# Optimization experiments

Measured on AMD Instinct MI355X. Metric: run time of the kernel, lower is better.

The kernel has to match this reference:

```python
import jax, jax.numpy as jnp
import numpy as np
from jax import lax

N_GAUSS = 8192
SEM_DIM = 32


def setup_inputs() -> dict:
    key = jax.random.key(0)
    k1, k2, k3, k4, k5 = jax.random.split(key, 5)
    H, W = 1024, 1024
    # centers sampled inside the view frustum of an identity-pose pinhole camera
    z = jax.random.uniform(k1, (N_GAUSS,), minval=0.5, maxval=6.0)
    xy = jax.random.uniform(k2, (N_GAUSS, 2), minval=-0.6, maxval=0.6) * z[:, None]
    centers = jnp.concatenate([xy, z[:, None]], axis=1).astype(jnp.float32)
    colors = jax.random.uniform(k3, (N_GAUSS, 3), dtype=jnp.float32)
    opacities = jax.random.uniform(k4, (N_GAUSS, 1), dtype=jnp.float32)
    sem_feats = jax.random.normal(k5, (N_GAUSS, SEM_DIM), dtype=jnp.float32) * 0.1
    camera_pose = jnp.eye(4, dtype=jnp.float32)
    fx = fy = 800.0
    camera_intrinsics = jnp.array([[fx, 0.0, W / 2.0], [0.0, fy, H / 2.0], [0.0, 0.0, 1.0]], dtype=jnp.float32)
    return {
        "centers": centers,
        "colors": colors,
        "opacities": opacities,
        "sem_feats": sem_feats,
        "camera_pose": camera_pose,
        "camera_intrinsics": camera_intrinsics,
        "H": H,
        "W": W,
    }


def reference(centers, colors, opacities, sem_feats, camera_pose, camera_intrinsics, H, W):
    # Differentiable point-splat alpha compositing (faithful to render_gaussians).
    # Torch recurrence per pixel: alpha_i = o_i * (1 - A), A += alpha_i
    # => transmittance before i equals prod_{j<i, same pixel, nearer depth}(1 - o_j).
    N = centers.shape[0]
    cam = centers @ camera_pose[:3, :3].T + camera_pose[:3, 3]  # (N,3)
    z = cam[:, 2]
    valid = z > 0.1
    proj = cam @ camera_intrinsics.T  # (N,3)
    denom = jnp.where(valid, proj[:, 2], 1.0)
    # .long() in torch truncates toward zero; astype(int32) matches for the kept range
    px = (proj[:, 0] / denom).astype(jnp.int32)
    py = (proj[:, 1] / denom).astype(jnp.int32)
    ok = valid & (px >= 0) & (px < W) & (py >= 0) & (py < H)
    pid = jnp.where(ok, py * W + px, H * W)  # invalid -> dump bucket
    o = jnp.where(ok, opacities[:, 0], 0.0)
    depth = jnp.where(ok, z, jnp.inf)
    # sort primarily by pixel, secondarily by depth (front-to-back within pixel)
    order = jnp.lexsort((depth, pid))
    pid_s = pid[order]
    o_s = o[order]
    feats = jnp.concatenate([colors, sem_feats], axis=1)[order]  # (N, 3+D)
    # segmented exclusive cumprod of (1 - o) in log space
    log_t = jnp.log1p(-jnp.clip(o_s, 0.0, 1.0 - 1e-7))
    csum = jnp.cumsum(log_t)
    excl = csum - log_t
    boundary = jnp.concatenate([jnp.array([True]), pid_s[1:] != pid_s[:-1]])
    start_idx = lax.cummax(jnp.where(boundary, jnp.arange(N), 0))
    T = jnp.exp(excl - excl[start_idx])  # transmittance before each splat
    alpha = o_s * T
    out_flat = jax.ops.segment_sum(alpha[:, None] * feats, pid_s, num_segments=H * W + 1)[: H * W]
    feat_dim = feats.shape[1]
    return out_flat.T.reshape(feat_dim, H, W)
```

## Files before the change

kernel.cpp:

```cpp
#include <hip/hip_runtime.h>
#include <stdint.h>

#define CT 4096

__global__ __launch_bounds__(256) void gs_zero_project_kernel(
        float* __restrict__ out, int n,
        const float* __restrict__ centers, const float* __restrict__ opac,
        const float* __restrict__ pose, const float* __restrict__ Km,
        const int* __restrict__ Hp, const int* __restrict__ Wp,
        unsigned long long* __restrict__ ws_keys, float* __restrict__ ws_o,
        int N) {
    int idx = blockIdx.x * blockDim.x + threadIdx.x;
    int stride = gridDim.x * blockDim.x;
    int n4 = n >> 2;
    float4* o4 = (float4*)out;
    float4 z = make_float4(0.f, 0.f, 0.f, 0.f);
    for (int i = idx; i < n4; i += stride) o4[i] = z;
    if (idx < (n & 3)) out[(n4 << 2) + idx] = 0.f;

    if (idx < N) {
        const int H = *Hp, W = *Wp;
        float x = centers[3 * idx], y = centers[3 * idx + 1], zc = centers[3 * idx + 2];
        float cxx = pose[0] * x + pose[1] * y + pose[2]  * zc + pose[3];
        float cyy = pose[4] * x + pose[5] * y + pose[6]  * zc + pose[7];
        float czz = pose[8] * x + pose[9] * y + pose[10] * zc + pose[11];
        bool valid = czz > 0.1f;
        float p0 = Km[0] * cxx + Km[1] * cyy + Km[2] * czz;
        float p1 = Km[3] * cxx + Km[4] * cyy + Km[5] * czz;
        float p2 = Km[6] * cxx + Km[7] * cyy + Km[8] * czz;
        float denom = valid ? p2 : 1.0f;
        int px = (int)(p0 / denom);
        int py = (int)(p1 / denom);
        bool ok = valid && px >= 0 && px < W && py >= 0 && py < H;
        unsigned int pid = ok ? (unsigned int)(py * W + px) : (unsigned int)(H * W);
        float depth = ok ? czz : __int_as_float(0x7f800000);
        ws_keys[idx] = ((unsigned long long)pid << 32) |
                       (unsigned long long)__float_as_uint(depth);
        ws_o[idx] = ok ? opac[idx] : 0.0f;
    }
}

__global__ __launch_bounds__(1024) void gs_splat_kernel(
        const unsigned long long* __restrict__ keys, const float* __restrict__ opacs,
        const float* __restrict__ colors, const float* __restrict__ sem,
        float* __restrict__ out, int N, int sem_dim, const int* __restrict__ Hp,
        const int* __restrict__ Wp) {
    __shared__ unsigned long long sk[CT];
    __shared__ float so[CT];

    const int t = threadIdx.x;
    const int lane = t & 63;
    const int wave = t >> 6;
    const int HW = (*Hp) * (*Wp);

    const int i = blockIdx.x * 16 + wave;
    unsigned long long ki = ~0ull;
    float oi = 0.0f;
    if (i < N) { ki = keys[i]; oi = opacs[i]; }
    const unsigned int pid_i = (unsigned int)(ki >> 32);

    float prod = 1.0f;
    for (int base = 0; base < N; base += CT) {
        const int tile = (N - base < CT) ? (N - base) : CT;
        __syncthreads();
        for (int j = t; j < tile; j += 1024) {
            sk[j] = keys[base + j];
            so[j] = opacs[base + j];
        }
        __syncthreads();
        for (int j = lane; j < tile; j += 64) {
            unsigned long long kj = sk[j];
            if ((unsigned int)(kj >> 32) == pid_i) {
                int gj = base + j;
                if (kj < ki || (kj == ki && gj < i)) {
                    prod *= 1.0f - fminf(fmaxf(so[j], 0.0f), 1.0f - 1e-7f);
                }
            }
        }
    }
    for (int off = 32; off > 0; off >>= 1) prod *= __shfl_xor(prod, off, 64);

    if (i >= N || pid_i >= (unsigned int)HW) return;
    float alpha = oi * prod;
    int fd = 3 + sem_dim;
    if (lane < fd) {
        float f = (lane < 3) ? colors[3 * i + lane] : sem[sem_dim * i + (lane - 3)];
        atomicAdd(&out[(size_t)lane * (size_t)HW + pid_i], alpha * f);
    }
}

extern "C" void kernel_launch(void* const* d_in, const int* in_sizes, int n_in,
                              void* d_out, int out_size, void* d_ws, size_t ws_size,
                              hipStream_t stream) {
    const float* centers = (const float*)d_in[0];
    const float* colors  = (const float*)d_in[1];
    const float* opac    = (const float*)d_in[2];
    const float* sem     = (const float*)d_in[3];
    const float* pose    = (const float*)d_in[4];
    const float* Km      = (const float*)d_in[5];
    const int*   Hp      = (const int*)d_in[6];
    const int*   Wp      = (const int*)d_in[7];

    int N = in_sizes[0] / 3;
    int sem_dim = in_sizes[3] / N;

    unsigned long long* ws_keys = (unsigned long long*)d_ws;
    float* ws_o = (float*)((char*)d_ws + (size_t)N * sizeof(unsigned long long));

    gs_zero_project_kernel<<<4096, 256, 0, stream>>>(
        (float*)d_out, out_size, centers, opac, pose, Km, Hp, Wp,
        ws_keys, ws_o, N);

    int blocks = (N + 15) / 16;
    gs_splat_kernel<<<blocks, 1024, 0, stream>>>(
        ws_keys, ws_o, colors, sem, (float*)d_out, N, sem_dim, Hp, Wp);
}
```

Baseline: 190.5 us.

## Stage all splat keys in LDS once and zero output via hipMemsetAsync

The splat kernel now copies all N sort keys into dynamically sized shared memory with a single barrier, replacing the tiled loop that synchronised twice per 4096-key tile. Opacity is read from global memory only when a key matches the pixel. Output zeroing moves from the projection kernel to hipMemsetAsync, and HW is computed on the host instead of being read from device memory. The cost is LDS use that scales with N (64 KB at N=8192), which can reduce occupancy and will fail for much larger N.

```diff
diff --git a/kernel.cpp b/kernel.cpp
--- a/kernel.cpp
+++ b/kernel.cpp
@@ -1,81 +1,60 @@
 #include <hip/hip_runtime.h>
 #include <stdint.h>
 
-#define CT 4096
-
-__global__ __launch_bounds__(256) void gs_zero_project_kernel(
-        float* __restrict__ out, int n,
+__global__ __launch_bounds__(256) void gs_project_kernel(
         const float* __restrict__ centers, const float* __restrict__ opac,
         const float* __restrict__ pose, const float* __restrict__ Km,
         const int* __restrict__ Hp, const int* __restrict__ Wp,
         unsigned long long* __restrict__ ws_keys, float* __restrict__ ws_o,
         int N) {
-    int idx = blockIdx.x * blockDim.x + threadIdx.x;
-    int stride = gridDim.x * blockDim.x;
-    int n4 = n >> 2;
-    float4* o4 = (float4*)out;
-    float4 z = make_float4(0.f, 0.f, 0.f, 0.f);
-    for (int i = idx; i < n4; i += stride) o4[i] = z;
-    if (idx < (n & 3)) out[(n4 << 2) + idx] = 0.f;
-
-    if (idx < N) {
-        const int H = *Hp, W = *Wp;
-        float x = centers[3 * idx], y = centers[3 * idx + 1], zc = centers[3 * idx + 2];
-        float cxx = pose[0] * x + pose[1] * y + pose[2]  * zc + pose[3];
-        float cyy = pose[4] * x + pose[5] * y + pose[6]  * zc + pose[7];
-        float czz = pose[8] * x + pose[9] * y + pose[10] * zc + pose[11];
-        bool valid = czz > 0.1f;
-        float p0 = Km[0] * cxx + Km[1] * cyy + Km[2] * czz;
-        float p1 = Km[3] * cxx + Km[4] * cyy + Km[5] * czz;
-        float p2 = Km[6] * cxx + Km[7] * cyy + Km[8] * czz;
-        float denom = valid ? p2 : 1.0f;
-        int px = (int)(p0 / denom);
-        int py = (int)(p1 / denom);
-        bool ok = valid && px >= 0 && px < W && py >= 0 && py < H;
-        unsigned int pid = ok ? (unsigned int)(py * W + px) : (unsigned int)(H * W);
-        float depth = ok ? czz : __int_as_float(0x7f800000);
-        ws_keys[idx] = ((unsigned long long)pid << 32) |
-                       (unsigned long long)__float_as_uint(depth);
-        ws_o[idx] = ok ? opac[idx] : 0.0f;
-    }
+    int i = blockIdx.x * blockDim.x + threadIdx.x;
+    if (i >= N) return;
+    const int H = *Hp, W = *Wp;
+    float x = centers[3 * i], y = centers[3 * i + 1], zc = centers[3 * i + 2];
+    float cxx = pose[0] * x + pose[1] * y + pose[2]  * zc + pose[3];
+    float cyy = pose[4] * x + pose[5] * y + pose[6]  * zc + pose[7];
+    float czz = pose[8] * x + pose[9] * y + pose[10] * zc + pose[11];
+    bool valid = czz > 0.1f;
+    float p0 = Km[0] * cxx + Km[1] * cyy + Km[2] * czz;
+    float p1 = Km[3] * cxx + Km[4] * cyy + Km[5] * czz;
+    float p2 = Km[6] * cxx + Km[7] * cyy + Km[8] * czz;
+    float denom = valid ? p2 : 1.0f;
+    int px = (int)(p0 / denom);
+    int py = (int)(p1 / denom);
+    bool ok = valid && px >= 0 && px < W && py >= 0 && py < H;
+    unsigned int pid = ok ? (unsigned int)(py * W + px) : (unsigned int)(H * W);
+    float depth = ok ? czz : __int_as_float(0x7f800000);
+    ws_keys[i] = ((unsigned long long)pid << 32) |
+                 (unsigned long long)__float_as_uint(depth);
+    ws_o[i] = ok ? opac[i] : 0.0f;
 }
 
 __global__ __launch_bounds__(1024) void gs_splat_kernel(
-        const unsigned long long* __restrict__ keys, const float* __restrict__ opacs,
+        const unsigned long long* __restrict__ keys,
+        const float* __restrict__ opacs,
         const float* __restrict__ colors, const float* __restrict__ sem,
-        float* __restrict__ out, int N, int sem_dim, const int* __restrict__ Hp,
-        const int* __restrict__ Wp) {
-    __shared__ unsigned long long sk[CT];
-    __shared__ float so[CT];
-
+        float* __restrict__ out, int N, int sem_dim, int HW) {
+    extern __shared__ unsigned long long sk[];
     const int t = threadIdx.x;
     const int lane = t & 63;
     const int wave = t >> 6;
-    const int HW = (*Hp) * (*Wp);
+    const int i = blockIdx.x * 16 + wave;
 
-    const int i = blockIdx.x * 16 + wave;
+    for (int j = t; j < N; j += 1024) sk[j] = keys[j];
+    __syncthreads();
+
     unsigned long long ki = ~0ull;
     float oi = 0.0f;
-    if (i < N) { ki = keys[i]; oi = opacs[i]; }
+    if (i < N) { ki = sk[i]; oi = opacs[i]; }
     const unsigned int pid_i = (unsigned int)(ki >> 32);
 
     float prod = 1.0f;
-    for (int base = 0; base < N; base += CT) {
-        const int tile = (N - base < CT) ? (N - base) : CT;
-        __syncthreads();
-        for (int j = t; j < tile; j += 1024) {
-            sk[j] = keys[base + j];
-            so[j] = opacs[base + j];
-        }
-        __syncthreads();
-        for (int j = lane; j < tile; j += 64) {
-            unsigned long long kj = sk[j];
-            if ((unsigned int)(kj >> 32) == pid_i) {
-                int gj = base + j;
-                if (kj < ki || (kj == ki && gj < i)) {
-                    prod *= 1.0f - fminf(fmaxf(so[j], 0.0f), 1.0f - 1e-7f);
-                }
-            }
+    for (int j = lane; j < N; j += 64) {
+        unsigned long long kj = sk[j];
+        if ((unsigned int)(kj >> 32) == pid_i &&
+            (kj < ki || (kj == ki && j < i))) {
+            float oj = opacs[j];
+            prod *= 1.0f - fminf(fmaxf(oj, 0.0f), 1.0f - 1e-7f);
         }
     }
     for (int off = 32; off > 0; off >>= 1) prod *= __shfl_xor(prod, off, 64);
@@ -103,15 +82,19 @@
 
     int N = in_sizes[0] / 3;
     int sem_dim = in_sizes[3] / N;
+    int fd = 3 + sem_dim;
+    int HW = out_size / fd;
 
     unsigned long long* ws_keys = (unsigned long long*)d_ws;
     float* ws_o = (float*)((char*)d_ws + (size_t)N * sizeof(unsigned long long));
 
-    gs_zero_project_kernel<<<4096, 256, 0, stream>>>(
-        (float*)d_out, out_size, centers, opac, pose, Km, Hp, Wp,
-        ws_keys, ws_o, N);
+    hipMemsetAsync(d_out, 0, (size_t)out_size * sizeof(float), stream);
+
+    gs_project_kernel<<<(N + 255) / 256, 256, 0, stream>>>(
+        centers, opac, pose, Km, Hp, Wp, ws_keys, ws_o, N);
 
     int blocks = (N + 15) / 16;
-    gs_splat_kernel<<<blocks, 1024, 0, stream>>>(
-        ws_keys, ws_o, colors, sem, (float*)d_out, N, sem_dim, Hp, Wp);
+    size_t lds = (size_t)N * sizeof(unsigned long long);
+    gs_splat_kernel<<<blocks, 1024, lds, stream>>>(
+        ws_keys, ws_o, colors, sem, (float*)d_out, N, sem_dim, HW);
 }
```

Result: no change. 190.1 us (-0.2%).
